# Kernel optimization log

Measured on AMD Instinct MI355X. Metric: run time of the kernel, lower is better.

Reference implementation:

```python
import jax, jax.numpy as jnp
import numpy as np

N, E, B = 50000, 400000, 64
N_INC, E_OUTC, U_INC, G_INC = 64, 64, 32, 64
H1A, H1B = 128, 64           # node_model_mlp1_hidden_sizes
H2 = 256                     # node_model_mlp2_hidden_sizes[0]
DIM_LH, DIM_L, N_OUTC = 128, 32, 64
LN_EPS = 1e-5

def _lin_init(key, din, dout):
    k1, k2 = jax.random.split(key)
    bound = 1.0 / np.sqrt(din)
    W = jax.random.uniform(k1, (din, dout), jnp.float32, -bound, bound)
    b = jax.random.uniform(k2, (dout,), jnp.float32, -bound, bound)
    return W, b

def setup_inputs() -> dict:
    key = jax.random.key(0)
    ks = jax.random.split(key, 16)
    x = jax.random.normal(ks[0], (N, N_INC), jnp.float32)
    edge_index = jax.random.randint(ks[1], (2, E), 0, N, jnp.int64)
    edge_attr = jax.random.normal(ks[2], (E, E_OUTC), jnp.float32)
    u = jax.random.normal(ks[3], (B, U_INC), jnp.float32)
    batch = jnp.sort(jax.random.randint(ks[4], (N,), 0, B, jnp.int64))
    goal = jax.random.normal(ks[5], (N, G_INC), jnp.float32)
    W1, b1 = _lin_init(ks[6], N_INC + E_OUTC, H1A)
    g1, be1 = jnp.ones((H1A,), jnp.float32), jnp.zeros((H1A,), jnp.float32)
    W2, b2 = _lin_init(ks[7], H1A, H1B)
    mlp2_inc = N_INC + H1B + U_INC
    W3, b3 = _lin_init(ks[8], mlp2_inc, H2)
    g3, be3 = jnp.ones((H2,), jnp.float32), jnp.zeros((H2,), jnp.float32)
    W4, b4 = _lin_init(ks[9], H2, DIM_LH)
    g4, be4 = jnp.ones((DIM_LH,), jnp.float32), jnp.zeros((DIM_LH,), jnp.float32)
    Wm, bm = _lin_init(ks[10], DIM_LH, DIM_L)
    Wv, bv = _lin_init(ks[11], DIM_LH, DIM_L)
    Wx, bx = _lin_init(ks[12], DIM_L, N_OUTC)
    return dict(x=x, edge_index=edge_index, edge_attr=edge_attr, u=u, batch=batch,
                goal=goal, W1=W1, b1=b1, g1=g1, be1=be1, W2=W2, b2=b2,
                W3=W3, b3=b3, g3=g3, be3=be3, W4=W4, b4=b4, g4=g4, be4=be4,
                Wm=Wm, bm=bm, Wv=Wv, bv=bv, Wx=Wx, bx=bx)

def _layernorm(h, g, b):
    mu = jnp.mean(h, axis=-1, keepdims=True)
    var = jnp.var(h, axis=-1, keepdims=True)
    return (h - mu) * jax.lax.rsqrt(var + LN_EPS) * g + b

def reference(x, edge_index, edge_attr, u, batch, goal,
              W1, b1, g1, be1, W2, b2,
              W3, b3, g3, be3, W4, b4, g4, be4,
              Wm, bm, Wv, bv, Wx, bx):
    row, col = edge_index[0], edge_index[1]
    # --- edge MLP: gather x[row], concat edge_attr, 2-layer MLP with LN+ReLU
    se = jnp.concatenate([x[row], edge_attr], axis=1)          # [E, n_inc+e_outc]
    h = jax.nn.relu(_layernorm(se @ W1 + b1, g1, be1)) @ W2 + b2  # [E, H1B]
    # --- scatter_mean over destination nodes
    sums = jax.ops.segment_sum(h, col, num_segments=N)          # [N, H1B]
    cnts = jax.ops.segment_sum(jnp.ones((E,), h.dtype), col, num_segments=N)
    aggs = sums / jnp.maximum(cnts, 1.0)[:, None]
    # --- node MLP 2
    z = jnp.concatenate([x, aggs, u[batch]], axis=1)            # [N, mlp2_inc]
    z = jax.nn.relu(_layernorm(z @ W3 + b3, g3, be3))
    z = jax.nn.relu(_layernorm(z @ W4 + b4, g4, be4))           # [N, DIM_LH]
    z_mu = z @ Wm + bm
    z_var = z @ Wv + bv                                         # log-variance
    eps = jax.random.normal(jax.random.key(42), z_mu.shape, z_mu.dtype)
    z_s = z_mu + eps * jnp.exp(0.5 * z_var)                     # reparameterize
    out = z_s @ Wx + bx                                         # [N, n_outc]
    return (out, z_mu, z_var)
```

## Files before the change

kernel.cpp:

```cpp
#include <hip/hip_runtime.h>

#define NN 50000
#define EE 400000
#define NB 49

typedef __attribute__((ext_vector_type(8))) short bf16x8;
typedef __attribute__((ext_vector_type(4))) float f32x4;

__device__ __forceinline__ void fma4(float4& a, float s, const float4& w){
  a.x = fmaf(s, w.x, a.x);
  a.y = fmaf(s, w.y, a.y);
  a.z = fmaf(s, w.z, a.z);
  a.w = fmaf(s, w.w, a.w);
}

__device__ __forceinline__ unsigned short f2bf(float f){
  unsigned u = __float_as_uint(f);
  unsigned r = (u + 0x7fffu + ((u >> 16) & 1u)) >> 16;
  return (unsigned short)r;
}

__device__ __forceinline__ bf16x8 cvt8(float4 lo, float4 hi){
  bf16x8 r;
  r[0]=(short)f2bf(lo.x); r[1]=(short)f2bf(lo.y); r[2]=(short)f2bf(lo.z); r[3]=(short)f2bf(lo.w);
  r[4]=(short)f2bf(hi.x); r[5]=(short)f2bf(hi.y); r[6]=(short)f2bf(hi.z); r[7]=(short)f2bf(hi.w);
  return r;
}

__device__ __forceinline__ unsigned rotl32(unsigned v, int d){ return (v<<d)|(v>>(32-d)); }

__device__ __forceinline__ float eps_at(unsigned idx){
  const unsigned k0 = 0u, k1 = 42u, k2 = 0x1BD11BDAu ^ 0u ^ 42u;
  unsigned x0 = 0u + k0, x1 = idx + k1;
  const int rotA[4] = {13,15,26,6};
  const int rotB[4] = {17,29,16,24};
  #pragma unroll
  for (int i=0;i<4;i++){ x0 += x1; x1 = rotl32(x1, rotA[i]); x1 ^= x0; }
  x0 += k1; x1 += k2 + 1u;
  #pragma unroll
  for (int i=0;i<4;i++){ x0 += x1; x1 = rotl32(x1, rotB[i]); x1 ^= x0; }
  x0 += k2; x1 += k0 + 2u;
  #pragma unroll
  for (int i=0;i<4;i++){ x0 += x1; x1 = rotl32(x1, rotA[i]); x1 ^= x0; }
  x0 += k0; x1 += k1 + 3u;
  #pragma unroll
  for (int i=0;i<4;i++){ x0 += x1; x1 = rotl32(x1, rotB[i]); x1 ^= x0; }
  x0 += k1; x1 += k2 + 4u;
  #pragma unroll
  for (int i=0;i<4;i++){ x0 += x1; x1 = rotl32(x1, rotA[i]); x1 ^= x0; }
  x0 += k2; x1 += k0 + 5u;
  unsigned bits = x0 ^ x1;
  float f = __uint_as_float((bits >> 9) | 0x3f800000u) - 1.0f;
  const float lo = -0.99999994f;
  float u = f * 2.0f + lo;
  u = fmaxf(u, lo);
  float w = -log1pf(-u*u);
  float p;
  if (w < 5.0f){
    w -= 2.5f;
    p = 2.81022636e-08f;
    p = fmaf(p,w, 3.43273939e-07f);
    p = fmaf(p,w,-3.5233877e-06f);
    p = fmaf(p,w,-4.39150654e-06f);
    p = fmaf(p,w, 0.00021858087f);
    p = fmaf(p,w,-0.00125372503f);
    p = fmaf(p,w,-0.00417768164f);
    p = fmaf(p,w, 0.246640727f);
    p = fmaf(p,w, 1.50140941f);
  } else {
    w = sqrtf(w) - 3.0f;
    p = -0.000200214257f;
    p = fmaf(p,w, 0.000100950558f);
    p = fmaf(p,w, 0.00134934322f);
    p = fmaf(p,w,-0.00367342844f);
    p = fmaf(p,w, 0.00573950773f);
    p = fmaf(p,w,-0.0076224613f);
    p = fmaf(p,w, 0.00943887047f);
    p = fmaf(p,w, 1.00167406f);
    p = fmaf(p,w, 2.83297682f);
  }
  return 1.41421356237f * (p * u);
}

__global__ __launch_bounds__(256) void k_prep_x(const float* __restrict__ x,
                                                unsigned short* __restrict__ xb){
  int t = blockIdx.x*256 + threadIdx.x;
  if (t < NN*64/8){
    const float4* p = (const float4*)(x + t*8);
    bf16x8 v = cvt8(p[0], p[1]);
    *(bf16x8*)(xb + t*8) = v;
  }
}

__global__ __launch_bounds__(256) void k_prep_w(const float* __restrict__ W1,
                                                const float* __restrict__ W2,
                                                unsigned short* __restrict__ W1T,
                                                unsigned short* __restrict__ W2T){
  for (int i = threadIdx.x; i < 128*128; i += 256){
    int n = i >> 7, k = i & 127;
    W1T[i] = f2bf(W1[k*128 + n]);
  }
  for (int i = threadIdx.x; i < 64*128; i += 256){
    int n = i >> 7, k = i & 127;
    W2T[i] = f2bf(W2[k*64 + n]);
  }
}

__global__ __launch_bounds__(256) void k_hist(const int* __restrict__ ei, int* __restrict__ cnt){
  int e = blockIdx.x*256 + threadIdx.x;
  if (e < EE) atomicAdd(&cnt[ei[EE + e]], 1);
}

__global__ __launch_bounds__(256) void k_scan1(const int* __restrict__ cnt,
                                               int* __restrict__ offs,
                                               int* __restrict__ partials){
  __shared__ int sdata[256];
  const int t = threadIdx.x, b = blockIdx.x;
  const int base = b*1024 + t*4;
  int v0 = (base+0 < NN) ? cnt[base+0] : 0;
  int v1 = (base+1 < NN) ? cnt[base+1] : 0;
  int v2 = (base+2 < NN) ? cnt[base+2] : 0;
  int v3 = (base+3 < NN) ? cnt[base+3] : 0;
  int tsum = v0+v1+v2+v3;
  sdata[t] = tsum;
  __syncthreads();
  for (int off=1; off<256; off<<=1){
    int add = (t >= off) ? sdata[t-off] : 0;
    __syncthreads();
    sdata[t] += add;
    __syncthreads();
  }
  int run = sdata[t] - tsum;
  if (base+0 < NN) offs[base+0] = run;  run += v0;
  if (base+1 < NN) offs[base+1] = run;  run += v1;
  if (base+2 < NN) offs[base+2] = run;  run += v2;
  if (base+3 < NN) offs[base+3] = run;
  if (t == 255) partials[b] = sdata[255];
}

__global__ __launch_bounds__(64) void k_scan2(int* __restrict__ partials){
  int l = threadIdx.x;
  int v = (l < NB) ? partials[l] : 0;
  int inc = v;
  #pragma unroll
  for (int off=1; off<64; off<<=1){
    int t = __shfl_up(inc, off);
    if (l >= off) inc += t;
  }
  if (l < NB) partials[l] = inc - v;
}

__global__ __launch_bounds__(256) void k_scan3(int* __restrict__ offs,
                                               const int* __restrict__ partials,
                                               int* __restrict__ cursor){
  const int t = threadIdx.x, b = blockIdx.x;
  const int base = b*1024 + t*4;
  int add = partials[b];
  #pragma unroll
  for (int k=0;k<4;k++){
    int i = base + k;
    if (i < NN){ int o = offs[i] + add; offs[i] = o; cursor[i] = o; }
  }
}

__global__ __launch_bounds__(256) void k_fill(const int* __restrict__ ei,
                                              int* __restrict__ cursor,
                                              int* __restrict__ epos){
  int e = blockIdx.x*256 + threadIdx.x;
  if (e < EE){
    int c = ei[EE + e];
    epos[e] = atomicAdd(&cursor[c], 1);
  }
}

#define H1STR 132
__global__ __launch_bounds__(256, 4) void k_edge(const int* __restrict__ ei,
    const float* __restrict__ ea,
    const unsigned short* __restrict__ xb,
    const unsigned short* __restrict__ W1T, const float* __restrict__ b1,
    const float* __restrict__ g1, const float* __restrict__ be1,
    const unsigned short* __restrict__ W2T, const float* __restrict__ b2,
    const int* __restrict__ epos,
    float* __restrict__ h_ws){
  __shared__ __align__(16) float h1[64*H1STR];
  __shared__ int rows_l[64];
  __shared__ int slot_l[64];
  const int tid  = threadIdx.x;
  const int base = blockIdx.x * 64;
  const int wv   = tid >> 6;
  const int lane = tid & 63;
  const int quad = lane >> 4;
  const int l16  = lane & 15;
  if (tid < 64) rows_l[tid] = ei[base + tid];
  if (tid >= 128 && tid < 192) slot_l[tid-128] = epos[base + tid - 128];
  __syncthreads();
  {
    int rw[4];
    #pragma unroll
    for (int m=0;m<4;m++) rw[m] = rows_l[m*16 + l16];
    f32x4 acc[4][2];
    #pragma unroll
    for (int m=0;m<4;m++){ acc[m][0] = (f32x4){0.f,0.f,0.f,0.f}; acc[m][1] = (f32x4){0.f,0.f,0.f,0.f}; }
    #pragma unroll
    for (int ks=0; ks<4; ks++){
      bf16x8 af[4];
      if (ks < 2){
        #pragma unroll
        for (int m=0;m<4;m++)
          af[m] = *(const bf16x8*)(xb + (size_t)rw[m]*64 + ks*32 + quad*8);
      } else {
        #pragma unroll
        for (int m=0;m<4;m++){
          const float* p = ea + (size_t)(base + m*16 + l16)*64 + (ks-2)*32 + quad*8;
          af[m] = cvt8(*(const float4*)p, *(const float4*)(p+4));
        }
      }
      bf16x8 bf0 = *(const bf16x8*)(W1T + (size_t)((2*wv+0)*16 + l16)*128 + ks*32 + quad*8);
      bf16x8 bf1 = *(const bf16x8*)(W1T + (size_t)((2*wv+1)*16 + l16)*128 + ks*32 + quad*8);
      #pragma unroll
      for (int m=0;m<4;m++){
        acc[m][0] = __builtin_amdgcn_mfma_f32_16x16x32_bf16(af[m], bf0, acc[m][0], 0, 0, 0);
        acc[m][1] = __builtin_amdgcn_mfma_f32_16x16x32_bf16(af[m], bf1, acc[m][1], 0, 0, 0);
      }
    }
    #pragma unroll
    for (int nl=0; nl<2; nl++){
      float b1c = b1[(2*wv+nl)*16 + l16];
      #pragma unroll
      for (int m=0;m<4;m++){
        #pragma unroll
        for (int r=0;r<4;r++)
          h1[(m*16 + quad*4 + r)*H1STR + (2*wv+nl)*16 + l16] = acc[m][nl][r] + b1c;
      }
    }
  }
  __syncthreads();
  {
    const float gA = g1[lane], gB = g1[lane+64];
    const float bA = be1[lane], bB = be1[lane+64];
    for (int r = wv*16; r < wv*16 + 16; ++r){
      float a = h1[r*H1STR + lane];
      float b = h1[r*H1STR + 64 + lane];
      float s = a + b, ss = fmaf(a,a,b*b);
      #pragma unroll
      for (int off=32; off; off>>=1){
        s  += __shfl_xor(s, off);
        ss += __shfl_xor(ss, off);
      }
      float mean = s * (1.0f/128.0f);
      float var  = ss * (1.0f/128.0f) - mean*mean;
      float inv = rsqrtf(var + 1e-5f);
      h1[r*H1STR + lane]      = fmaxf(fmaf((a-mean)*inv, gA, bA), 0.f);
      h1[r*H1STR + 64 + lane] = fmaxf(fmaf((b-mean)*inv, gB, bB), 0.f);
    }
  }
  __syncthreads();
  {
    f32x4 acc2[4];
    #pragma unroll
    for (int m=0;m<4;m++) acc2[m] = (f32x4){0.f,0.f,0.f,0.f};
    #pragma unroll
    for (int ks=0; ks<4; ks++){
      bf16x8 bfr = *(const bf16x8*)(W2T + (size_t)(wv*16 + l16)*128 + ks*32 + quad*8);
      #pragma unroll
      for (int m=0;m<4;m++){
        const float* p = h1 + (m*16 + l16)*H1STR + ks*32 + quad*8;
        bf16x8 af = cvt8(*(const float4*)p, *(const float4*)(p+4));
        acc2[m] = __builtin_amdgcn_mfma_f32_16x16x32_bf16(af, bfr, acc2[m], 0, 0, 0);
      }
    }
    float b2c = b2[wv*16 + l16];
    #pragma unroll
    for (int m=0;m<4;m++){
      #pragma unroll
      for (int r=0;r<4;r++)
        h_ws[(size_t)slot_l[m*16 + quad*4 + r]*64 + wv*16 + l16] = acc2[m][r] + b2c;
    }
  }
}

#define T2STR 132
#define ZSSTR 36
__global__ __launch_bounds__(256, 3) void k_node(const float* __restrict__ x,
    const float* __restrict__ u, const int* __restrict__ batch,
    const float* __restrict__ h_ws, const int* __restrict__ cnt,
    const int* __restrict__ offs,
    const float* __restrict__ W3, const float* __restrict__ b3,
    const float* __restrict__ g3, const float* __restrict__ be3,
    const float* __restrict__ W4, const float* __restrict__ b4,
    const float* __restrict__ g4, const float* __restrict__ be4,
    const float* __restrict__ Wm, const float* __restrict__ bm,
    const float* __restrict__ Wv, const float* __restrict__ bv,
    const float* __restrict__ Wx, const float* __restrict__ bx,
    float* __restrict__ out){
  __shared__ __align__(16) float zS[32*160];
  __shared__ __align__(16) float h3S[32*256];
  const int tid = threadIdx.x;
  const int base = blockIdx.x * 32;
  #pragma unroll
  for (int i=0;i<2;i++){
    int l = tid + 256*i;
    int r = l >> 4, c4 = (l & 15) * 4;
    int n = base + r;
    float4 v = make_float4(0.f,0.f,0.f,0.f);
    if (n < NN) v = *(const float4*)(x + (size_t)n*64 + c4);
    *(float4*)(zS + r*160 + c4) = v;
  }
  {
    int r = tid >> 3, c4 = (tid & 7) * 4;
    int n = base + r;
    float4 v = make_float4(0.f,0.f,0.f,0.f);
    if (n < NN) v = *(const float4*)(u + (size_t)batch[n]*32 + c4);
    *(float4*)(zS + r*160 + 128 + c4) = v;
  }
  {
    int r = tid >> 3, p = tid & 7;
    int n = base + r;
    float4 a0 = make_float4(0.f,0.f,0.f,0.f), a1 = a0;
    int deg = 0;
    if (n < NN){
      deg = cnt[n];
      const float* hp = h_ws + (size_t)offs[n]*64 + p*8;
      int j = 0;
      for (; j + 2 <= deg; j += 2){
        float4 v0 = *(const float4*)(hp);
        float4 v1 = *(const float4*)(hp + 4);
        float4 w0 = *(const float4*)(hp + 64);
        float4 w1 = *(const float4*)(hp + 68);
        hp += 128;
        a0.x += v0.x; a0.y += v0.y; a0.z += v0.z; a0.w += v0.w;
        a1.x += v1.x; a1.y += v1.y; a1.z += v1.z; a1.w += v1.w;
        a0.x += w0.x; a0.y += w0.y; a0.z += w0.z; a0.w += w0.w;
        a1.x += w1.x; a1.y += w1.y; a1.z += w1.z; a1.w += w1.w;
      }
      if (j < deg){
        float4 v0 = *(const float4*)(hp);
        float4 v1 = *(const float4*)(hp + 4);
        a0.x += v0.x; a0.y += v0.y; a0.z += v0.z; a0.w += v0.w;
        a1.x += v1.x; a1.y += v1.y; a1.z += v1.z; a1.w += v1.w;
      }
    }
    float rc = 1.0f / fmaxf((float)deg, 1.0f);
    a0.x*=rc; a0.y*=rc; a0.z*=rc; a0.w*=rc;
    a1.x*=rc; a1.y*=rc; a1.z*=rc; a1.w*=rc;
    *(float4*)(zS + r*160 + 64 + p*8)     = a0;
    *(float4*)(zS + r*160 + 64 + p*8 + 4) = a1;
  }
  __syncthreads();
  {
    const int jq = tid & 63, rb = tid >> 6;
    float4 acc[8];
    #pragma unroll
    for (int r=0;r<8;r++) acc[r] = make_float4(0.f,0.f,0.f,0.f);
    for (int k=0;k<160;k+=4){
      float4 w0 = *(const float4*)(W3 + (k+0)*256 + 4*jq);
      float4 w1 = *(const float4*)(W3 + (k+1)*256 + 4*jq);
      float4 w2 = *(const float4*)(W3 + (k+2)*256 + 4*jq);
      float4 w3v= *(const float4*)(W3 + (k+3)*256 + 4*jq);
      #pragma unroll
      for (int r=0;r<8;r++){
        float4 z = *(const float4*)(zS + (rb*8+r)*160 + k);
        fma4(acc[r], z.x, w0); fma4(acc[r], z.y, w1);
        fma4(acc[r], z.z, w2); fma4(acc[r], z.w, w3v);
      }
    }
    float4 bb  = *(const float4*)(b3 + 4*jq);
    float4 gg  = *(const float4*)(g3 + 4*jq);
    float4 bet = *(const float4*)(be3 + 4*jq);
    #pragma unroll
    for (int r=0;r<8;r++){
      float4 v = acc[r];
      v.x += bb.x; v.y += bb.y; v.z += bb.z; v.w += bb.w;
      float s  = v.x + v.y + v.z + v.w;
      float ss = fmaf(v.x,v.x, fmaf(v.y,v.y, fmaf(v.z,v.z, v.w*v.w)));
      #pragma unroll
      for (int off=32; off; off>>=1){ s += __shfl_xor(s,off); ss += __shfl_xor(ss,off); }
      float mean = s * (1.0f/256.0f);
      float inv  = rsqrtf(ss*(1.0f/256.0f) - mean*mean + 1e-5f);
      float4 o;
      o.x = fmaxf(fmaf((v.x-mean)*inv, gg.x, bet.x), 0.f);
      o.y = fmaxf(fmaf((v.y-mean)*inv, gg.y, bet.y), 0.f);
      o.z = fmaxf(fmaf((v.z-mean)*inv, gg.z, bet.z), 0.f);
      o.w = fmaxf(fmaf((v.w-mean)*inv, gg.w, bet.w), 0.f);
      *(float4*)(h3S + (rb*8+r)*256 + 4*jq) = o;
    }
  }
  __syncthreads();
  {
    const int jq = tid & 31, rb = tid >> 5;
    float4 acc[4];
    #pragma unroll
    for (int r=0;r<4;r++) acc[r] = make_float4(0.f,0.f,0.f,0.f);
    for (int k=0;k<256;k+=4){
      float4 w0 = *(const float4*)(W4 + (k+0)*128 + 4*jq);
      float4 w1 = *(const float4*)(W4 + (k+1)*128 + 4*jq);
      float4 w2 = *(const float4*)(W4 + (k+2)*128 + 4*jq);
      float4 w3 = *(const float4*)(W4 + (k+3)*128 + 4*jq);
      #pragma unroll
      for (int r=0;r<4;r++){
        float4 z = *(const float4*)(h3S + (rb*4+r)*256 + k);
        fma4(acc[r], z.x, w0); fma4(acc[r], z.y, w1);
        fma4(acc[r], z.z, w2); fma4(acc[r], z.w, w3);
      }
    }
    float4 bb  = *(const float4*)(b4 + 4*jq);
    float4 gg  = *(const float4*)(g4 + 4*jq);
    float4 bet = *(const float4*)(be4 + 4*jq);
    #pragma unroll
    for (int r=0;r<4;r++){
      float4 v = acc[r];
      v.x += bb.x; v.y += bb.y; v.z += bb.z; v.w += bb.w;
      float s  = v.x + v.y + v.z + v.w;
      float ss = fmaf(v.x,v.x, fmaf(v.y,v.y, fmaf(v.z,v.z, v.w*v.w)));
      #pragma unroll
      for (int off=16; off; off>>=1){ s += __shfl_xor(s,off); ss += __shfl_xor(ss,off); }
      float mean = s * (1.0f/128.0f);
      float inv  = rsqrtf(ss*(1.0f/128.0f) - mean*mean + 1e-5f);
      float4 o;
      o.x = fmaxf(fmaf((v.x-mean)*inv, gg.x, bet.x), 0.f);
      o.y = fmaxf(fmaf((v.y-mean)*inv, gg.y, bet.y), 0.f);
      o.z = fmaxf(fmaf((v.z-mean)*inv, gg.z, bet.z), 0.f);
      o.w = fmaxf(fmaf((v.w-mean)*inv, gg.w, bet.w), 0.f);
      *(float4*)(zS + (rb*4+r)*T2STR + 4*jq) = o;
    }
  }
  __syncthreads();
  {
    const int jq = tid & 15, rb = tid >> 4;
    const float* Wp = (jq < 8) ? Wm : Wv;
    const int cq = (jq & 7) * 4;
    float4 acc[2];
    #pragma unroll
    for (int r=0;r<2;r++) acc[r] = make_float4(0.f,0.f,0.f,0.f);
    for (int k=0;k<128;k+=4){
      float4 w0 = *(const float4*)(Wp + (k+0)*32 + cq);
      float4 w1 = *(const float4*)(Wp + (k+1)*32 + cq);
      float4 w2 = *(const float4*)(Wp + (k+2)*32 + cq);
      float4 w3 = *(const float4*)(Wp + (k+3)*32 + cq);
      #pragma unroll
      for (int r=0;r<2;r++){
        float4 z = *(const float4*)(zS + (rb*2+r)*T2STR + k);
        fma4(acc[r], z.x, w0); fma4(acc[r], z.y, w1);
        fma4(acc[r], z.z, w2); fma4(acc[r], z.w, w3);
      }
    }
    const float* bp = (jq < 8) ? bm : bv;
    float4 bb = *(const float4*)(bp + cq);
    const long long sec = (jq < 8) ? (long long)NN*64 : ((long long)NN*64 + (long long)NN*32);
    #pragma unroll
    for (int r=0;r<2;r++){
      float4 v = acc[r];
      v.x += bb.x; v.y += bb.y; v.z += bb.z; v.w += bb.w;
      int rr = rb*2 + r;
      *(float4*)(h3S + rr*64 + ((jq<8)?0:32) + cq) = v;
      int n = base + rr;
      if (n < NN) *(float4*)(out + sec + (long long)n*32 + cq) = v;
    }
  }
  __syncthreads();
  #pragma unroll
  for (int i=0;i<4;i++){
    int l = tid + 256*i;
    int r = l >> 5, jj = l & 31;
    float mu = h3S[r*64 + jj];
    float lv = h3S[r*64 + 32 + jj];
    unsigned idx = (unsigned)((base + r)*32 + jj);
    float e = eps_at(idx);
    zS[r*ZSSTR + jj] = fmaf(e, expf(0.5f*lv), mu);
  }
  __syncthreads();
  {
    const int jq = tid & 15, rb = tid >> 4;
    float4 acc[2];
    #pragma unroll
    for (int r=0;r<2;r++) acc[r] = make_float4(0.f,0.f,0.f,0.f);
    for (int k=0;k<32;k+=4){
      float4 w0 = *(const float4*)(Wx + (k+0)*64 + 4*jq);
      float4 w1 = *(const float4*)(Wx + (k+1)*64 + 4*jq);
      float4 w2 = *(const float4*)(Wx + (k+2)*64 + 4*jq);
      float4 w3 = *(const float4*)(Wx + (k+3)*64 + 4*jq);
      #pragma unroll
      for (int r=0;r<2;r++){
        float4 z = *(const float4*)(zS + (rb*2+r)*ZSSTR + k);
        fma4(acc[r], z.x, w0); fma4(acc[r], z.y, w1);
        fma4(acc[r], z.z, w2); fma4(acc[r], z.w, w3);
      }
    }
    float4 bb = *(const float4*)(bx + 4*jq);
    #pragma unroll
    for (int r=0;r<2;r++){
      int n = base + rb*2 + r;
      if (n < NN){
        float4 v = acc[r];
        v.x += bb.x; v.y += bb.y; v.z += bb.z; v.w += bb.w;
        *(float4*)(out + (long long)n*64 + 4*jq) = v;
      }
    }
  }
}

extern "C" void kernel_launch(void* const* d_in, const int* in_sizes, int n_in,
                              void* d_out, int out_size, void* d_ws, size_t ws_size,
                              hipStream_t stream) {
  const float* x     = (const float*)d_in[0];
  const int*   ei    = (const int*)d_in[1];
  const float* ea    = (const float*)d_in[2];
  const float* u     = (const float*)d_in[3];
  const int*   batch = (const int*)d_in[4];
  const float* W1 = (const float*)d_in[6];
  const float* b1 = (const float*)d_in[7];
  const float* g1 = (const float*)d_in[8];
  const float* be1= (const float*)d_in[9];
  const float* W2 = (const float*)d_in[10];
  const float* b2 = (const float*)d_in[11];
  const float* W3 = (const float*)d_in[12];
  const float* b3 = (const float*)d_in[13];
  const float* g3 = (const float*)d_in[14];
  const float* be3= (const float*)d_in[15];
  const float* W4 = (const float*)d_in[16];
  const float* b4 = (const float*)d_in[17];
  const float* g4 = (const float*)d_in[18];
  const float* be4= (const float*)d_in[19];
  const float* Wm = (const float*)d_in[20];
  const float* bm = (const float*)d_in[21];
  const float* Wv = (const float*)d_in[22];
  const float* bv = (const float*)d_in[23];
  const float* Wx = (const float*)d_in[24];
  const float* bx = (const float*)d_in[25];

  char* W = (char*)d_ws;
  size_t off = 0;
  float* h_ws = (float*)(W + off);  off += (size_t)EE*64*4;
  int* cnt      = (int*)(W + off);  off += (size_t)NN*4;
  int* offs     = (int*)(W + off);  off += (size_t)NN*4;
  int* cursor   = (int*)(W + off);  off += (size_t)NN*4;
  int* epos     = (int*)(W + off);  off += (size_t)EE*4;
  int* partials = (int*)(W + off);  off += 256;
  unsigned short* xb  = (unsigned short*)(W + off); off += (size_t)NN*64*2;
  unsigned short* W1T = (unsigned short*)(W + off); off += 128*128*2;
  unsigned short* W2T = (unsigned short*)(W + off); off += 64*128*2;
  float* out = (float*)d_out;

  hipMemsetAsync(cnt, 0, (size_t)NN*sizeof(int), stream);

  k_prep_x<<<(NN*64/8 + 255)/256, 256, 0, stream>>>(x, xb);
  k_prep_w<<<1, 256, 0, stream>>>(W1, W2, W1T, W2T);
  k_hist <<<(EE+255)/256, 256, 0, stream>>>(ei, cnt);
  k_scan1<<<NB, 256, 0, stream>>>(cnt, offs, partials);
  k_scan2<<<1, 64, 0, stream>>>(partials);
  k_scan3<<<NB, 256, 0, stream>>>(offs, partials, cursor);
  k_fill <<<(EE+255)/256, 256, 0, stream>>>(ei, cursor, epos);

  k_edge<<<EE/64, 256, 0, stream>>>(ei, ea, xb, W1T, b1, g1, be1, W2T, b2, epos, h_ws);
  k_node<<<(NN+31)/32, 256, 0, stream>>>(x, u, batch, h_ws, cnt, offs,
                                         W3,b3,g3,be3, W4,b4,g4,be4,
                                         Wm,bm, Wv,bv, Wx,bx, out);
}
```

Before: 575.0 us.

## Run node MLP W3/W4 GEMMs on MFMA with split-bf16 hi/lo precision

```diff
diff --git a/kernel.cpp b/kernel.cpp
--- a/kernel.cpp
+++ b/kernel.cpp
@@ -25,6 +25,30 @@
   r[0]=(short)f2bf(lo.x); r[1]=(short)f2bf(lo.y); r[2]=(short)f2bf(lo.z); r[3]=(short)f2bf(lo.w);
   r[4]=(short)f2bf(hi.x); r[5]=(short)f2bf(hi.y); r[6]=(short)f2bf(hi.z); r[7]=(short)f2bf(hi.w);
   return r;
+}
+
+__device__ __forceinline__ unsigned packhl(float v){
+  unsigned hi = f2bf(v);
+  float fh = __uint_as_float(hi << 16);
+  unsigned lo = f2bf(v - fh);
+  return (hi << 16) | lo;
+}
+
+__device__ __forceinline__ uint4 pack4(float4 v){
+  uint4 p;
+  p.x = packhl(v.x); p.y = packhl(v.y); p.z = packhl(v.z); p.w = packhl(v.w);
+  return p;
+}
+
+__device__ __forceinline__ void unpack8(uint4 p0, uint4 p1, bf16x8& hi, bf16x8& lo){
+  hi[0]=(short)(p0.x>>16); lo[0]=(short)(p0.x & 0xffffu);
+  hi[1]=(short)(p0.y>>16); lo[1]=(short)(p0.y & 0xffffu);
+  hi[2]=(short)(p0.z>>16); lo[2]=(short)(p0.z & 0xffffu);
+  hi[3]=(short)(p0.w>>16); lo[3]=(short)(p0.w & 0xffffu);
+  hi[4]=(short)(p1.x>>16); lo[4]=(short)(p1.x & 0xffffu);
+  hi[5]=(short)(p1.y>>16); lo[5]=(short)(p1.y & 0xffffu);
+  hi[6]=(short)(p1.z>>16); lo[6]=(short)(p1.z & 0xffffu);
+  hi[7]=(short)(p1.w>>16); lo[7]=(short)(p1.w & 0xffffu);
 }
 
 __device__ __forceinline__ unsigned rotl32(unsigned v, int d){ return (v<<d)|(v>>(32-d)); }
@@ -106,6 +130,33 @@
   }
 }
 
+__global__ __launch_bounds__(256) void k_prep_w34(const float* __restrict__ W3,
+                                                  const float* __restrict__ W4,
+                                                  unsigned short* __restrict__ W3Th,
+                                                  unsigned short* __restrict__ W3Tl,
+                                                  unsigned short* __restrict__ W4Th,
+                                                  unsigned short* __restrict__ W4Tl){
+  int b = blockIdx.x;
+  if (b < 256){
+    int n = b;
+    for (int k = threadIdx.x; k < 160; k += 256){
+      float w = W3[k*256 + n];
+      unsigned h = f2bf(w);
+      float fh = __uint_as_float(h << 16);
+      W3Th[n*160 + k] = (unsigned short)h;
+      W3Tl[n*160 + k] = f2bf(w - fh);
+    }
+  } else {
+    int n = b - 256;
+    int k = threadIdx.x;
+    float w = W4[k*128 + n];
+    unsigned h = f2bf(w);
+    float fh = __uint_as_float(h << 16);
+    W4Th[n*256 + k] = (unsigned short)h;
+    W4Tl[n*256 + k] = f2bf(w - fh);
+  }
+}
+
 __global__ __launch_bounds__(256) void k_hist(const int* __restrict__ ei, int* __restrict__ cnt){
   int e = blockIdx.x*256 + threadIdx.x;
   if (e < EE) atomicAdd(&cnt[ei[EE + e]], 1);
@@ -281,22 +332,35 @@
 
 #define T2STR 132
 #define ZSSTR 36
+#define ZPSTR 164
+#define H3STR 260
 __global__ __launch_bounds__(256, 3) void k_node(const float* __restrict__ x,
     const float* __restrict__ u, const int* __restrict__ batch,
     const float* __restrict__ h_ws, const int* __restrict__ cnt,
     const int* __restrict__ offs,
-    const float* __restrict__ W3, const float* __restrict__ b3,
+    const unsigned short* __restrict__ W3Th, const unsigned short* __restrict__ W3Tl,
+    const float* __restrict__ b3,
     const float* __restrict__ g3, const float* __restrict__ be3,
-    const float* __restrict__ W4, const float* __restrict__ b4,
+    const unsigned short* __restrict__ W4Th, const unsigned short* __restrict__ W4Tl,
+    const float* __restrict__ b4,
     const float* __restrict__ g4, const float* __restrict__ be4,
     const float* __restrict__ Wm, const float* __restrict__ bm,
     const float* __restrict__ Wv, const float* __restrict__ bv,
     const float* __restrict__ Wx, const float* __restrict__ bx,
     float* __restrict__ out){
-  __shared__ __align__(16) float zS[32*160];
-  __shared__ __align__(16) float h3S[32*256];
+  __shared__ __align__(16) char arena[(32*H3STR + 32*ZPSTR)*4];
+  float*    h3f = (float*)arena;
+  unsigned* h3p = (unsigned*)arena;
+  unsigned* zPK = (unsigned*)(arena + 32*H3STR*4);
+  float*    t2S = (float*)(arena + 32*H3STR*4);
+
   const int tid = threadIdx.x;
   const int base = blockIdx.x * 32;
+  const int wv   = tid >> 6;
+  const int lane = tid & 63;
+  const int quad = lane >> 4;
+  const int l16  = lane & 15;
+
   #pragma unroll
   for (int i=0;i<2;i++){
     int l = tid + 256*i;
@@ -304,14 +368,14 @@
     int n = base + r;
     float4 v = make_float4(0.f,0.f,0.f,0.f);
     if (n < NN) v = *(const float4*)(x + (size_t)n*64 + c4);
-    *(float4*)(zS + r*160 + c4) = v;
+    *(uint4*)(zPK + r*ZPSTR + c4) = pack4(v);
   }
   {
     int r = tid >> 3, c4 = (tid & 7) * 4;
     int n = base + r;
     float4 v = make_float4(0.f,0.f,0.f,0.f);
     if (n < NN) v = *(const float4*)(u + (size_t)batch[n]*32 + c4);
-    *(float4*)(zS + r*160 + 128 + c4) = v;
+    *(uint4*)(zPK + r*ZPSTR + 128 + c4) = pack4(v);
   }
   {
     int r = tid >> 3, p = tid & 7;
@@ -343,34 +407,50 @@
     float rc = 1.0f / fmaxf((float)deg, 1.0f);
     a0.x*=rc; a0.y*=rc; a0.z*=rc; a0.w*=rc;
     a1.x*=rc; a1.y*=rc; a1.z*=rc; a1.w*=rc;
-    *(float4*)(zS + r*160 + 64 + p*8)     = a0;
-    *(float4*)(zS + r*160 + 64 + p*8 + 4) = a1;
-  }
-  __syncthreads();
-  {
-    const int jq = tid & 63, rb = tid >> 6;
-    float4 acc[8];
-    #pragma unroll
-    for (int r=0;r<8;r++) acc[r] = make_float4(0.f,0.f,0.f,0.f);
-    for (int k=0;k<160;k+=4){
-      float4 w0 = *(const float4*)(W3 + (k+0)*256 + 4*jq);
-      float4 w1 = *(const float4*)(W3 + (k+1)*256 + 4*jq);
-      float4 w2 = *(const float4*)(W3 + (k+2)*256 + 4*jq);
-      float4 w3v= *(const float4*)(W3 + (k+3)*256 + 4*jq);
-      #pragma unroll
-      for (int r=0;r<8;r++){
-        float4 z = *(const float4*)(zS + (rb*8+r)*160 + k);
-        fma4(acc[r], z.x, w0); fma4(acc[r], z.y, w1);
-        fma4(acc[r], z.z, w2); fma4(acc[r], z.w, w3v);
-      }
-    }
-    float4 bb  = *(const float4*)(b3 + 4*jq);
-    float4 gg  = *(const float4*)(g3 + 4*jq);
-    float4 bet = *(const float4*)(be3 + 4*jq);
+    *(uint4*)(zPK + r*ZPSTR + 64 + p*8)     = pack4(a0);
+    *(uint4*)(zPK + r*ZPSTR + 64 + p*8 + 4) = pack4(a1);
+  }
+  __syncthreads();
+  {
+    const int mt = wv & 1;
+    const int ng = wv >> 1;
+    f32x4 acc[8];
+    #pragma unroll
+    for (int i=0;i<8;i++) acc[i] = (f32x4){0.f,0.f,0.f,0.f};
+    #pragma unroll
+    for (int ks=0; ks<5; ks++){
+      const unsigned* ap = zPK + (mt*16 + l16)*ZPSTR + ks*32 + quad*8;
+      uint4 p0 = *(const uint4*)ap;
+      uint4 p1 = *(const uint4*)(ap + 4);
+      bf16x8 ah, al;
+      unpack8(p0, p1, ah, al);
+      #pragma unroll
+      for (int i=0;i<8;i++){
+        int nt = ng*8 + i;
+        bf16x8 bh = *(const bf16x8*)(W3Th + (size_t)(nt*16 + l16)*160 + ks*32 + quad*8);
+        bf16x8 bl = *(const bf16x8*)(W3Tl + (size_t)(nt*16 + l16)*160 + ks*32 + quad*8);
+        acc[i] = __builtin_amdgcn_mfma_f32_16x16x32_bf16(ah, bh, acc[i], 0, 0, 0);
+        acc[i] = __builtin_amdgcn_mfma_f32_16x16x32_bf16(al, bh, acc[i], 0, 0, 0);
+        acc[i] = __builtin_amdgcn_mfma_f32_16x16x32_bf16(ah, bl, acc[i], 0, 0, 0);
+      }
+    }
+    #pragma unroll
+    for (int i=0;i<8;i++){
+      int nt = ng*8 + i;
+      float bc = b3[nt*16 + l16];
+      #pragma unroll
+      for (int r=0;r<4;r++)
+        h3f[(mt*16 + quad*4 + r)*H3STR + nt*16 + l16] = acc[i][r] + bc;
+    }
+  }
+  __syncthreads();
+  {
+    float4 gg  = *(const float4*)(g3 + lane*4);
+    float4 bet = *(const float4*)(be3 + lane*4);
     #pragma unroll
     for (int r=0;r<8;r++){
-      float4 v = acc[r];
-      v.x += bb.x; v.y += bb.y; v.z += bb.z; v.w += bb.w;
+      int row = wv*8 + r;
+      float4 v = *(const float4*)(h3f + row*H3STR + lane*4);
       float s  = v.x + v.y + v.z + v.w;
       float ss = fmaf(v.x,v.x, fmaf(v.y,v.y, fmaf(v.z,v.z, v.w*v.w)));
       #pragma unroll
@@ -382,34 +462,51 @@
       o.y = fmaxf(fmaf((v.y-mean)*inv, gg.y, bet.y), 0.f);
       o.z = fmaxf(fmaf((v.z-mean)*inv, gg.z, bet.z), 0.f);
       o.w = fmaxf(fmaf((v.w-mean)*inv, gg.w, bet.w), 0.f);
-      *(float4*)(h3S + (rb*8+r)*256 + 4*jq) = o;
+      *(uint4*)(h3p + row*H3STR + lane*4) = pack4(o);
+    }
+  }
+  __syncthreads();
+  {
+    const int mt = wv & 1;
+    const int np = wv >> 1;
+    f32x4 acc[4];
+    #pragma unroll
+    for (int i=0;i<4;i++) acc[i] = (f32x4){0.f,0.f,0.f,0.f};
+    #pragma unroll
+    for (int ks=0; ks<8; ks++){
+      const unsigned* ap = h3p + (mt*16 + l16)*H3STR + ks*32 + quad*8;
+      uint4 p0 = *(const uint4*)ap;
+      uint4 p1 = *(const uint4*)(ap + 4);
+      bf16x8 ah, al;
+      unpack8(p0, p1, ah, al);
+      #pragma unroll
+      for (int i=0;i<4;i++){
+        int nt = np*4 + i;
+        bf16x8 bh = *(const bf16x8*)(W4Th + (size_t)(nt*16 + l16)*256 + ks*32 + quad*8);
+        bf16x8 bl = *(const bf16x8*)(W4Tl + (size_t)(nt*16 + l16)*256 + ks*32 + quad*8);
+        acc[i] = __builtin_amdgcn_mfma_f32_16x16x32_bf16(ah, bh, acc[i], 0, 0, 0);
+        acc[i] = __builtin_amdgcn_mfma_f32_16x16x32_bf16(al, bh, acc[i], 0, 0, 0);
+        acc[i] = __builtin_amdgcn_mfma_f32_16x16x32_bf16(ah, bl, acc[i], 0, 0, 0);
+      }
+    }
+    #pragma unroll
+    for (int i=0;i<4;i++){
+      int nt = np*4 + i;
+      float bc = b4[nt*16 + l16];
+      #pragma unroll
+      for (int r=0;r<4;r++)
+        t2S[(mt*16 + quad*4 + r)*T2STR + nt*16 + l16] = acc[i][r] + bc;
     }
   }
   __syncthreads();
   {
     const int jq = tid & 31, rb = tid >> 5;
-    float4 acc[4];
-    #pragma unroll
-    for (int r=0;r<4;r++) acc[r] = make_float4(0.f,0.f,0.f,0.f);
-    for (int k=0;k<256;k+=4){
-      float4 w0 = *(const float4*)(W4 + (k+0)*128 + 4*jq);
-      float4 w1 = *(const float4*)(W4 + (k+1)*128 + 4*jq);
-      float4 w2 = *(const float4*)(W4 + (k+2)*128 + 4*jq);
-      float4 w3 = *(const float4*)(W4 + (k+3)*128 + 4*jq);
-      #pragma unroll
-      for (int r=0;r<4;r++){
-        float4 z = *(const float4*)(h3S + (rb*4+r)*256 + k);
-        fma4(acc[r], z.x, w0); fma4(acc[r], z.y, w1);
-        fma4(acc[r], z.z, w2); fma4(acc[r], z.w, w3);
-      }
-    }
-    float4 bb  = *(const float4*)(b4 + 4*jq);
     float4 gg  = *(const float4*)(g4 + 4*jq);
     float4 bet = *(const float4*)(be4 + 4*jq);
     #pragma unroll
     for (int r=0;r<4;r++){
-      float4 v = acc[r];
-      v.x += bb.x; v.y += bb.y; v.z += bb.z; v.w += bb.w;
+      int row = rb*4 + r;
+      float4 v = *(const float4*)(t2S + row*T2STR + 4*jq);
       float s  = v.x + v.y + v.z + v.w;
       float ss = fmaf(v.x,v.x, fmaf(v.y,v.y, fmaf(v.z,v.z, v.w*v.w)));
       #pragma unroll
@@ -421,7 +518,7 @@
       o.y = fmaxf(fmaf((v.y-mean)*inv, gg.y, bet.y), 0.f);
       o.z = fmaxf(fmaf((v.z-mean)*inv, gg.z, bet.z), 0.f);
       o.w = fmaxf(fmaf((v.w-mean)*inv, gg.w, bet.w), 0.f);
-      *(float4*)(zS + (rb*4+r)*T2STR + 4*jq) = o;
+      *(float4*)(t2S + row*T2STR + 4*jq) = o;
     }
   }
   __syncthreads();
@@ -439,7 +536,7 @@
       float4 w3 = *(const float4*)(Wp + (k+3)*32 + cq);
       #pragma unroll
       for (int r=0;r<2;r++){
-        float4 z = *(const float4*)(zS + (rb*2+r)*T2STR + k);
+        float4 z = *(const float4*)(t2S + (rb*2+r)*T2STR + k);
         fma4(acc[r], z.x, w0); fma4(acc[r], z.y, w1);
         fma4(acc[r], z.z, w2); fma4(acc[r], z.w, w3);
       }
@@ -452,7 +549,7 @@
       float4 v = acc[r];
       v.x += bb.x; v.y += bb.y; v.z += bb.z; v.w += bb.w;
       int rr = rb*2 + r;
-      *(float4*)(h3S + rr*64 + ((jq<8)?0:32) + cq) = v;
+      *(float4*)(h3f + rr*64 + ((jq<8)?0:32) + cq) = v;
       int n = base + rr;
       if (n < NN) *(float4*)(out + sec + (long long)n*32 + cq) = v;
     }
@@ -462,11 +559,11 @@
   for (int i=0;i<4;i++){
     int l = tid + 256*i;
     int r = l >> 5, jj = l & 31;
-    float mu = h3S[r*64 + jj];
-    float lv = h3S[r*64 + 32 + jj];
+    float mu = h3f[r*64 + jj];
+    float lv = h3f[r*64 + 32 + jj];
     unsigned idx = (unsigned)((base + r)*32 + jj);
     float e = eps_at(idx);
-    zS[r*ZSSTR + jj] = fmaf(e, expf(0.5f*lv), mu);
+    t2S[r*ZSSTR + jj] = fmaf(e, expf(0.5f*lv), mu);
   }
   __syncthreads();
   {
@@ -481,7 +578,7 @@
       float4 w3 = *(const float4*)(Wx + (k+3)*64 + 4*jq);
       #pragma unroll
       for (int r=0;r<2;r++){
-        float4 z = *(const float4*)(zS + (rb*2+r)*ZSSTR + k);
+        float4 z = *(const float4*)(t2S + (rb*2+r)*ZSSTR + k);
         fma4(acc[r], z.x, w0); fma4(acc[r], z.y, w1);
         fma4(acc[r], z.z, w2); fma4(acc[r], z.w, w3);
       }
@@ -539,12 +636,17 @@
   unsigned short* xb  = (unsigned short*)(W + off); off += (size_t)NN*64*2;
   unsigned short* W1T = (unsigned short*)(W + off); off += 128*128*2;
   unsigned short* W2T = (unsigned short*)(W + off); off += 64*128*2;
+  unsigned short* W3Th = (unsigned short*)(W + off); off += 256*160*2;
+  unsigned short* W3Tl = (unsigned short*)(W + off); off += 256*160*2;
+  unsigned short* W4Th = (unsigned short*)(W + off); off += 128*256*2;
+  unsigned short* W4Tl = (unsigned short*)(W + off); off += 128*256*2;
   float* out = (float*)d_out;
 
   hipMemsetAsync(cnt, 0, (size_t)NN*sizeof(int), stream);
 
   k_prep_x<<<(NN*64/8 + 255)/256, 256, 0, stream>>>(x, xb);
   k_prep_w<<<1, 256, 0, stream>>>(W1, W2, W1T, W2T);
+  k_prep_w34<<<384, 256, 0, stream>>>(W3, W4, W3Th, W3Tl, W4Th, W4Tl);
   k_hist <<<(EE+255)/256, 256, 0, stream>>>(ei, cnt);
   k_scan1<<<NB, 256, 0, stream>>>(cnt, offs, partials);
   k_scan2<<<1, 64, 0, stream>>>(partials);
@@ -553,6 +655,7 @@
 
   k_edge<<<EE/64, 256, 0, stream>>>(ei, ea, xb, W1T, b1, g1, be1, W2T, b2, epos, h_ws);
   k_node<<<(NN+31)/32, 256, 0, stream>>>(x, u, batch, h_ws, cnt, offs,
-                                         W3,b3,g3,be3, W4,b4,g4,be4,
+                                         W3Th, W3Tl, b3, g3, be3,
+                                         W4Th, W4Tl, b4, g4, be4,
                                          Wm,bm, Wv,bv, Wx,bx, out);
 }
```

New measurement: 572.3 us. No clear change (-0.5%).
